# Kernel optimization log

Hardware: AMD Instinct MI355X
Metric: run time of the kernel (lower is better)

## Reference

```python
import jax, jax.numpy as jnp
import numpy as np

B = 2048        # batch
C = 4           # number of constraint matrices per sample
NRIS = 100      # physical RIS elements (theta dim)
MN = 16         # N_t * N_r
DIN = 303
DOUT = 200 + 4 * MN  # 264
THRESH_W = 10.0 ** (-120.0 / 10.0) / 1000.0  # 1e-15


def _init_linear(key, fan_in, fan_out):
    kw, _ = jax.random.split(key)
    W = jax.random.normal(kw, (fan_in, fan_out), dtype=jnp.float32) * (1.0 / np.sqrt(fan_in))
    b = jnp.zeros((fan_out,), dtype=jnp.float32)
    return W, b


def setup_inputs() -> dict:
    key = jax.random.key(0)
    ks = jax.random.split(key, 8)
    sample1 = jax.random.normal(ks[0], (B, DIN), dtype=jnp.float32)
    T_real = jax.random.normal(ks[1], (B, C, NRIS, NRIS), dtype=jnp.float32)
    T_imag = jax.random.normal(ks[2], (B, C, NRIS, NRIS), dtype=jnp.float32)
    W1, b1 = _init_linear(ks[3], DIN, 1024)
    W2, b2 = _init_linear(ks[4], 1024, 1024)
    W3, b3 = _init_linear(ks[5], 1024, 512)
    W4, b4 = _init_linear(ks[6], 512, DOUT)
    return {"sample1": sample1, "T_real": T_real, "T_imag": T_imag,
            "W1": W1, "b1": b1, "W2": W2, "b2": b2,
            "W3": W3, "b3": b3, "W4": W4, "b4": b4}


def reference(sample1, T_real, T_imag, W1, b1, W2, b2, W3, b3, W4, b4):
    # --- f1 MLP: 303 -> 1024 -> 1024 -> 512 -> 264 ---
    h = jax.nn.relu(sample1 @ W1 + b1)
    h = jax.nn.relu(h @ W2 + b2)
    h = jax.nn.relu(h @ W3 + b3)
    theta1 = h @ W4 + b4  # [B, 264]

    # --- precoder normalization: F <- F * sqrt(2 / F^H F) ---
    F1 = theta1[:, 200:200 + MN] + 1j * theta1[:, 200 + MN:200 + 2 * MN]      # [B, 16]
    F2 = theta1[:, 200 + 2 * MN:200 + 3 * MN] + 1j * theta1[:, 200 + 3 * MN:]  # [B, 16]
    F1 = F1 * jnp.sqrt(2.0 / jnp.sum(jnp.abs(F1) ** 2, axis=-1, keepdims=True))
    F2 = F2 * jnp.sqrt(2.0 / jnp.sum(jnp.abs(F2) ** 2, axis=-1, keepdims=True))

    # --- unit-modulus RIS phases ---
    theta = theta1[:, 0:NRIS] + 1j * theta1[:, NRIS:2 * NRIS]  # [B, 100]
    theta = theta / jnp.abs(theta)

    # --- ProjectRIS (batched): CCC_c = Re(theta^H (T_c / thr) theta), rescale if max > 1 ---
    T = T_real + 1j * T_imag  # [B, C, 100, 100]
    quad = jnp.einsum("bn,bcnm,bm->bc", jnp.conj(theta), T, theta)
    CCC = jnp.real(quad) / jnp.float32(THRESH_W)  # [B, C]
    mx = jnp.max(CCC, axis=1)  # [B]
    # scale = sqrt(1/mx) if mx > 1 else 1  ==  rsqrt(max(mx, 1))
    scale = jax.lax.rsqrt(jnp.maximum(mx, 1.0))
    theta_hat = theta * scale[:, None]

    # --- write back into theta1 layout ---
    out = jnp.concatenate([
        jnp.real(theta_hat), jnp.imag(theta_hat),
        jnp.real(F1), jnp.imag(F1),
        jnp.real(F2), jnp.imag(F2),
    ], axis=1)  # [B, 264]
    return out
```

## Files before the change

kernel.cpp:

```cpp
#include <hip/hip_runtime.h>
#include <math.h>

#define BATCH 2048
#define NRIS  100
#define MN    16
#define DIN   303
#define DOUT  264
#define TH1_LD 320

typedef short     bf16x8 __attribute__((ext_vector_type(8)));
typedef float     f32x4  __attribute__((ext_vector_type(4)));
typedef unsigned short u16;

__device__ __forceinline__ u16 f2bf(float x) {
    unsigned u = __float_as_uint(x);
    unsigned r = (u + 0x7fffu + ((u >> 16) & 1u)) >> 16;
    return (u16)r;
}
__device__ __forceinline__ float bf2f(u16 h) {
    return __uint_as_float(((unsigned)h) << 16);
}

__device__ __forceinline__ void gload_lds16(const void* g, void* lds) {
    __builtin_amdgcn_global_load_lds(
        (const __attribute__((address_space(1))) unsigned int*)g,
        (__attribute__((address_space(3))) unsigned int*)lds, 16, 0, 0);
}

template <int BM, int BN, bool RELU, bool SPLIT>
__global__ __launch_bounds__(256) void gemm_bf16x3(
    const u16* __restrict__ Ahi, const u16* __restrict__ Alo,
    const u16* __restrict__ Bhi, const u16* __restrict__ Blo,
    const float* __restrict__ bias, int Nb,
    float* __restrict__ Cf, u16* __restrict__ Chi, u16* __restrict__ Clo,
    int M, int N, int Kp)
{
    constexpr int WR = BM / 2, WC = BN / 2;
    constexpr int FM = WR / 16, FN = WC / 16;
    constexpr int IA = BM / 32;
    constexpr int IB = BN / 32;

    __shared__ __align__(16) short As[2][BM][64];
    __shared__ __align__(16) short Bs[2][BN][64];

    const int tid = threadIdx.x;
    const int w  = tid >> 6, l = tid & 63;
    const int lg = l >> 4, lx = l & 15, l7 = l & 7;
    const int bm = blockIdx.x * BM, bn = blockIdx.y * BN;
    const int wrow = (w >> 1) * WR, wcol = (w & 1) * WC;
    const int nt = Kp / 32;

    auto stage = [&](int k0, int buf) {
#pragma unroll
        for (int i = 0; i < IA; ++i) {
            int fi = (w * IA + i) * 64 + l;
            int r = fi >> 3, p = fi & 7, q = p ^ (r & 7);
            const u16* src = (q < 4)
                ? Ahi + (size_t)(bm + r) * Kp + k0 + q * 8
                : Alo + (size_t)(bm + r) * Kp + k0 + (q - 4) * 8;
            gload_lds16(src, &As[buf][0][0] + (size_t)(w * IA + i) * 512);
        }
#pragma unroll
        for (int i = 0; i < IB; ++i) {
            int fi = (w * IB + i) * 64 + l;
            int r = fi >> 3, p = fi & 7, q = p ^ (r & 7);
            const u16* src = (q < 4)
                ? Bhi + (size_t)(bn + r) * Kp + k0 + q * 8
                : Blo + (size_t)(bn + r) * Kp + k0 + (q - 4) * 8;
            gload_lds16(src, &Bs[buf][0][0] + (size_t)(w * IB + i) * 512);
        }
    };

    f32x4 acc[FM][FN];
#pragma unroll
    for (int i = 0; i < FM; ++i)
#pragma unroll
        for (int j = 0; j < FN; ++j) acc[i][j] = (f32x4){0.f, 0.f, 0.f, 0.f};

    stage(0, 0);
    __syncthreads();

    for (int t = 0; t < nt; ++t) {
        int cur = t & 1, nxt = cur ^ 1;
        if (t + 1 < nt) stage((t + 1) * 32, nxt);

        bf16x8 ah[FM], al[FM], bh[FN], bl[FN];
#pragma unroll
        for (int fm = 0; fm < FM; ++fm) {
            const short* base = &As[cur][wrow + fm * 16 + lx][0];
            ah[fm] = *(const bf16x8*)(base + ((lg ^ l7) << 3));
            al[fm] = *(const bf16x8*)(base + (((lg + 4) ^ l7) << 3));
        }
#pragma unroll
        for (int fn = 0; fn < FN; ++fn) {
            const short* base = &Bs[cur][wcol + fn * 16 + lx][0];
            bh[fn] = *(const bf16x8*)(base + ((lg ^ l7) << 3));
            bl[fn] = *(const bf16x8*)(base + (((lg + 4) ^ l7) << 3));
        }
#pragma unroll
        for (int fm = 0; fm < FM; ++fm)
#pragma unroll
            for (int fn = 0; fn < FN; ++fn) {
                acc[fm][fn] = __builtin_amdgcn_mfma_f32_16x16x32_bf16(
                    ah[fm], bh[fn], acc[fm][fn], 0, 0, 0);
                acc[fm][fn] = __builtin_amdgcn_mfma_f32_16x16x32_bf16(
                    ah[fm], bl[fn], acc[fm][fn], 0, 0, 0);
                acc[fm][fn] = __builtin_amdgcn_mfma_f32_16x16x32_bf16(
                    al[fm], bh[fn], acc[fm][fn], 0, 0, 0);
            }
        __syncthreads();
    }

#pragma unroll
    for (int fm = 0; fm < FM; ++fm)
#pragma unroll
        for (int fn = 0; fn < FN; ++fn) {
            int colg = bn + wcol + fn * 16 + lx;
            float bb = (colg < Nb) ? bias[colg] : 0.f;
#pragma unroll
            for (int r = 0; r < 4; ++r) {
                int rowg = bm + wrow + fm * 16 + lg * 4 + r;
                float v = acc[fm][fn][r] + bb;
                if (RELU) v = fmaxf(v, 0.f);
                if constexpr (SPLIT) {
                    u16 h = f2bf(v);
                    size_t o = (size_t)rowg * N + colg;
                    Chi[o] = h;
                    Clo[o] = f2bf(v - bf2f(h));
                } else {
                    Cf[(size_t)rowg * N + colg] = v;
                }
            }
        }
}

__global__ __launch_bounds__(256) void convtr_kernel(
    const float* __restrict__ W, u16* __restrict__ BThi, u16* __restrict__ BTlo,
    int K, int N, int Kp, int Np)
{
    __shared__ float T[64][65];
    int k0 = blockIdx.x * 64, n0 = blockIdx.y * 64;
    int c  = threadIdx.x & 63, r4 = threadIdx.x >> 6;
#pragma unroll
    for (int i = 0; i < 16; ++i) {
        int r = r4 * 16 + i;
        float v = 0.f;
        if (k0 + r < K && n0 + c < N) v = W[(size_t)(k0 + r) * N + n0 + c];
        T[r][c] = v;
    }
    __syncthreads();
#pragma unroll
    for (int i = 0; i < 16; ++i) {
        int nr = r4 * 16 + i;
        float v = T[c][nr];
        u16 h = f2bf(v);
        size_t o = (size_t)(n0 + nr) * Kp + k0 + c;
        BThi[o] = h;
        BTlo[o] = f2bf(v - bf2f(h));
    }
}

__global__ __launch_bounds__(256) void convpad_kernel(
    const float* __restrict__ X, u16* __restrict__ Hi, u16* __restrict__ Lo,
    int K, int Kp)
{
    int b = blockIdx.x;
    for (int k = threadIdx.x; k < Kp; k += 256) {
        float v = (k < K) ? X[(size_t)b * K + k] : 0.f;
        u16 h = f2bf(v);
        Hi[(size_t)b * Kp + k] = h;
        Lo[(size_t)b * Kp + k] = f2bf(v - bf2f(h));
    }
}

__global__ __launch_bounds__(128) void theta_prep_kernel(
    const float* __restrict__ th1, float* __restrict__ thU,
    float* __restrict__ out)
{
    int b   = blockIdx.x;
    int tid = threadIdx.x;
    const float* row = th1 + (size_t)b * TH1_LD;
    __shared__ float sc[2];

    if (tid == 112) {
        float s = 0.f;
        for (int j = 0; j < MN; ++j) {
            float fr = row[200 + j], fi = row[200 + MN + j];
            s += fr * fr + fi * fi;
        }
        sc[0] = sqrtf(2.f / s);
    } else if (tid == 113) {
        float s = 0.f;
        for (int j = 0; j < MN; ++j) {
            float fr = row[200 + 2 * MN + j], fi = row[200 + 3 * MN + j];
            s += fr * fr + fi * fi;
        }
        sc[1] = sqrtf(2.f / s);
    }

    if (tid < NRIS) {
        float re = row[tid], im = row[NRIS + tid];
        float r  = sqrtf(re * re + im * im);
        thU[(size_t)b * 200 + tid]        = re / r;
        thU[(size_t)b * 200 + NRIS + tid] = im / r;
    }
    __syncthreads();
    if (tid < 32) {
        int j = tid & 15, h = tid >> 4;
        out[(size_t)b * DOUT + 200 + h * MN + j]          = row[200 + h * MN + j] * sc[0];
        out[(size_t)b * DOUT + 200 + 2 * MN + h * MN + j] = row[200 + 2 * MN + h * MN + j] * sc[1];
    }
}

__global__ __launch_bounds__(256) void quadfin_kernel(
    const float* __restrict__ Tr, const float* __restrict__ Ti,
    const float* __restrict__ thU, float* __restrict__ out)
{
    int b   = blockIdx.x;
    int tid = threadIdx.x;

    __shared__ __align__(16) float sA[NRIS];
    __shared__ __align__(16) float sB[NRIS];
    if (tid < 200) {
        float v = thU[(size_t)b * 200 + tid];
        if (tid < NRIS) sA[tid] = v;
        else            sB[tid - NRIS] = v;
    }
    __syncthreads();

    const float4* R0 = (const float4*)(Tr + (size_t)b * 4 * (NRIS * NRIS));
    const float4* I0 = (const float4*)(Ti + (size_t)b * 4 * (NRIS * NRIS));

    float acc0 = 0.f, acc1 = 0.f, acc2 = 0.f, acc3 = 0.f;
    int n = tid / 25;
    int m = tid - n * 25;
    for (int j = tid; j < 2500; j += 256) {
        float an = sA[n], bn = sB[n];
        float4 am = *(const float4*)&sA[m * 4];
        float4 bm = *(const float4*)&sB[m * 4];
        float4 tR, tI;
        tR.x = an * am.x + bn * bm.x;  tI.x = bn * am.x - an * bm.x;
        tR.y = an * am.y + bn * bm.y;  tI.y = bn * am.y - an * bm.y;
        tR.z = an * am.z + bn * bm.z;  tI.z = bn * am.z - an * bm.z;
        tR.w = an * am.w + bn * bm.w;  tI.w = bn * am.w - an * bm.w;

        float4 r0 = R0[j],            i0 = I0[j];
        float4 r1 = R0[2500 + j],     i1 = I0[2500 + j];
        float4 r2 = R0[5000 + j],     i2 = I0[5000 + j];
        float4 r3 = R0[7500 + j],     i3 = I0[7500 + j];

        acc0 += r0.x * tR.x + r0.y * tR.y + r0.z * tR.z + r0.w * tR.w
              + i0.x * tI.x + i0.y * tI.y + i0.z * tI.z + i0.w * tI.w;
        acc1 += r1.x * tR.x + r1.y * tR.y + r1.z * tR.z + r1.w * tR.w
              + i1.x * tI.x + i1.y * tI.y + i1.z * tI.z + i1.w * tI.w;
        acc2 += r2.x * tR.x + r2.y * tR.y + r2.z * tR.z + r2.w * tR.w
              + i2.x * tI.x + i2.y * tI.y + i2.z * tI.z + i2.w * tI.w;
        acc3 += r3.x * tR.x + r3.y * tR.y + r3.z * tR.z + r3.w * tR.w
              + i3.x * tI.x + i3.y * tI.y + i3.z * tI.z + i3.w * tI.w;

        n += 10; m += 6;
        if (m >= 25) { m -= 25; ++n; }
    }

    int wave = tid >> 6, lane = tid & 63;
    for (int off = 32; off > 0; off >>= 1) {
        acc0 += __shfl_down(acc0, off, 64);
        acc1 += __shfl_down(acc1, off, 64);
        acc2 += __shfl_down(acc2, off, 64);
        acc3 += __shfl_down(acc3, off, 64);
    }
    __shared__ float ws4[4][4];
    if (lane == 0) {
        ws4[wave][0] = acc0; ws4[wave][1] = acc1;
        ws4[wave][2] = acc2; ws4[wave][3] = acc3;
    }
    __syncthreads();

    __shared__ float sc;
    if (tid == 0) {
        float mx = -1e30f;
#pragma unroll
        for (int c = 0; c < 4; ++c) {
            float s = ws4[0][c] + ws4[1][c] + ws4[2][c] + ws4[3][c];
            mx = fmaxf(mx, s);
        }
        mx *= 1e15f;
        sc = 1.f / sqrtf(fmaxf(mx, 1.0f));
    }
    __syncthreads();
    if (tid < NRIS) {
        out[(size_t)b * DOUT + tid]        = sA[tid] * sc;
        out[(size_t)b * DOUT + NRIS + tid] = sB[tid] * sc;
    }
}

extern "C" void kernel_launch(void* const* d_in, const int* in_sizes, int n_in,
                              void* d_out, int out_size, void* d_ws, size_t ws_size,
                              hipStream_t stream)
{
    const float* sample1 = (const float*)d_in[0];
    const float* T_real  = (const float*)d_in[1];
    const float* T_imag  = (const float*)d_in[2];
    const float* W1 = (const float*)d_in[3];
    const float* b1 = (const float*)d_in[4];
    const float* W2 = (const float*)d_in[5];
    const float* b2 = (const float*)d_in[6];
    const float* W3 = (const float*)d_in[7];
    const float* b3 = (const float*)d_in[8];
    const float* W4 = (const float*)d_in[9];
    const float* b4 = (const float*)d_in[10];
    float* out = (float*)d_out;

    char* p = (char*)d_ws;
    auto take = [&](size_t bytes) { char* q = p; p += bytes; return q; };
    u16* Shi   = (u16*)take((size_t)BATCH * 320 * 2);
    u16* Slo   = (u16*)take((size_t)BATCH * 320 * 2);
    u16* BT1hi = (u16*)take((size_t)1024 * 320 * 2);
    u16* BT1lo = (u16*)take((size_t)1024 * 320 * 2);
    u16* BT2hi = (u16*)take((size_t)1024 * 1024 * 2);
    u16* BT2lo = (u16*)take((size_t)1024 * 1024 * 2);
    u16* BT3hi = (u16*)take((size_t)512 * 1024 * 2);
    u16* BT3lo = (u16*)take((size_t)512 * 1024 * 2);
    u16* BT4hi = (u16*)take((size_t)320 * 512 * 2);
    u16* BT4lo = (u16*)take((size_t)320 * 512 * 2);
    u16* h1hi  = (u16*)take((size_t)BATCH * 1024 * 2);
    u16* h1lo  = (u16*)take((size_t)BATCH * 1024 * 2);
    u16* h2hi  = (u16*)take((size_t)BATCH * 1024 * 2);
    u16* h2lo  = (u16*)take((size_t)BATCH * 1024 * 2);
    u16* h3hi  = (u16*)take((size_t)BATCH * 512 * 2);
    u16* h3lo  = (u16*)take((size_t)BATCH * 512 * 2);
    float* th1 = (float*)take((size_t)BATCH * TH1_LD * 4);
    float* thU = (float*)take((size_t)BATCH * 200 * 4);

    dim3 blk(256);

    convpad_kernel<<<dim3(BATCH), blk, 0, stream>>>(sample1, Shi, Slo, DIN, 320);
    convtr_kernel<<<dim3(320 / 64, 1024 / 64), blk, 0, stream>>>(
        W1, BT1hi, BT1lo, DIN, 1024, 320, 1024);
    convtr_kernel<<<dim3(1024 / 64, 1024 / 64), blk, 0, stream>>>(
        W2, BT2hi, BT2lo, 1024, 1024, 1024, 1024);
    convtr_kernel<<<dim3(1024 / 64, 512 / 64), blk, 0, stream>>>(
        W3, BT3hi, BT3lo, 1024, 512, 1024, 512);
    convtr_kernel<<<dim3(512 / 64, 320 / 64), blk, 0, stream>>>(
        W4, BT4hi, BT4lo, 512, 264, 512, 320);

    gemm_bf16x3<64, 64, true, true><<<dim3(32, 16), blk, 0, stream>>>(
        Shi, Slo, BT1hi, BT1lo, b1, 1024, nullptr, h1hi, h1lo, BATCH, 1024, 320);
    gemm_bf16x3<64, 64, true, true><<<dim3(32, 16), blk, 0, stream>>>(
        h1hi, h1lo, BT2hi, BT2lo, b2, 1024, nullptr, h2hi, h2lo, BATCH, 1024, 1024);
    gemm_bf16x3<32, 64, true, true><<<dim3(64, 8), blk, 0, stream>>>(
        h2hi, h2lo, BT3hi, BT3lo, b3, 512, nullptr, h3hi, h3lo, BATCH, 512, 1024);
    gemm_bf16x3<32, 64, false, false><<<dim3(64, 5), blk, 0, stream>>>(
        h3hi, h3lo, BT4hi, BT4lo, b4, DOUT, th1, nullptr, nullptr, BATCH, TH1_LD, 512);

    theta_prep_kernel<<<dim3(BATCH), dim3(128), 0, stream>>>(th1, thU, out);
    quadfin_kernel<<<dim3(BATCH), blk, 0, stream>>>(T_real, T_imag, thU, out);
}
```

Measured before the change: 739.7 us.

## Widen GEMM K-tile, merge conversion kernels, fuse theta prep into quad kernel

```diff
diff --git a/kernel.cpp b/kernel.cpp
--- a/kernel.cpp
+++ b/kernel.cpp
@@ -37,36 +37,36 @@
 {
     constexpr int WR = BM / 2, WC = BN / 2;
     constexpr int FM = WR / 16, FN = WC / 16;
-    constexpr int IA = BM / 32;
-    constexpr int IB = BN / 32;
-
-    __shared__ __align__(16) short As[2][BM][64];
-    __shared__ __align__(16) short Bs[2][BN][64];
+    constexpr int IA = BM / 16;
+    constexpr int IB = BN / 16;
+
+    __shared__ __align__(16) short As[2][BM][128];
+    __shared__ __align__(16) short Bs[2][BN][128];
 
     const int tid = threadIdx.x;
     const int w  = tid >> 6, l = tid & 63;
-    const int lg = l >> 4, lx = l & 15, l7 = l & 7;
+    const int lg = l >> 4, lx = l & 15;
     const int bm = blockIdx.x * BM, bn = blockIdx.y * BN;
     const int wrow = (w >> 1) * WR, wcol = (w & 1) * WC;
-    const int nt = Kp / 32;
+    const int nt = Kp / 64;
 
     auto stage = [&](int k0, int buf) {
 #pragma unroll
         for (int i = 0; i < IA; ++i) {
             int fi = (w * IA + i) * 64 + l;
-            int r = fi >> 3, p = fi & 7, q = p ^ (r & 7);
-            const u16* src = (q < 4)
+            int r = fi >> 4, p = fi & 15, q = p ^ (r & 15);
+            const u16* src = (q < 8)
                 ? Ahi + (size_t)(bm + r) * Kp + k0 + q * 8
-                : Alo + (size_t)(bm + r) * Kp + k0 + (q - 4) * 8;
+                : Alo + (size_t)(bm + r) * Kp + k0 + (q - 8) * 8;
             gload_lds16(src, &As[buf][0][0] + (size_t)(w * IA + i) * 512);
         }
 #pragma unroll
         for (int i = 0; i < IB; ++i) {
             int fi = (w * IB + i) * 64 + l;
-            int r = fi >> 3, p = fi & 7, q = p ^ (r & 7);
-            const u16* src = (q < 4)
+            int r = fi >> 4, p = fi & 15, q = p ^ (r & 15);
+            const u16* src = (q < 8)
                 ? Bhi + (size_t)(bn + r) * Kp + k0 + q * 8
-                : Blo + (size_t)(bn + r) * Kp + k0 + (q - 4) * 8;
+                : Blo + (size_t)(bn + r) * Kp + k0 + (q - 8) * 8;
             gload_lds16(src, &Bs[buf][0][0] + (size_t)(w * IB + i) * 512);
         }
     };
@@ -82,32 +82,39 @@
 
     for (int t = 0; t < nt; ++t) {
         int cur = t & 1, nxt = cur ^ 1;
-        if (t + 1 < nt) stage((t + 1) * 32, nxt);
-
-        bf16x8 ah[FM], al[FM], bh[FN], bl[FN];
-#pragma unroll
-        for (int fm = 0; fm < FM; ++fm) {
-            const short* base = &As[cur][wrow + fm * 16 + lx][0];
-            ah[fm] = *(const bf16x8*)(base + ((lg ^ l7) << 3));
-            al[fm] = *(const bf16x8*)(base + (((lg + 4) ^ l7) << 3));
-        }
-#pragma unroll
-        for (int fn = 0; fn < FN; ++fn) {
-            const short* base = &Bs[cur][wcol + fn * 16 + lx][0];
-            bh[fn] = *(const bf16x8*)(base + ((lg ^ l7) << 3));
-            bl[fn] = *(const bf16x8*)(base + (((lg + 4) ^ l7) << 3));
-        }
-#pragma unroll
-        for (int fm = 0; fm < FM; ++fm)
+        if (t + 1 < nt) stage((t + 1) * 64, nxt);
+
+#pragma unroll
+        for (int s = 0; s < 2; ++s) {
+            bf16x8 ah[FM], al[FM], bh[FN], bl[FN];
+#pragma unroll
+            for (int fm = 0; fm < FM; ++fm) {
+                int row = wrow + fm * 16 + lx;
+                const short* base = &As[cur][row][0];
+                int r15 = row & 15;
+                ah[fm] = *(const bf16x8*)(base + (((s * 4 + lg) ^ r15) << 3));
+                al[fm] = *(const bf16x8*)(base + (((8 + s * 4 + lg) ^ r15) << 3));
+            }
 #pragma unroll
             for (int fn = 0; fn < FN; ++fn) {
-                acc[fm][fn] = __builtin_amdgcn_mfma_f32_16x16x32_bf16(
-                    ah[fm], bh[fn], acc[fm][fn], 0, 0, 0);
-                acc[fm][fn] = __builtin_amdgcn_mfma_f32_16x16x32_bf16(
-                    ah[fm], bl[fn], acc[fm][fn], 0, 0, 0);
-                acc[fm][fn] = __builtin_amdgcn_mfma_f32_16x16x32_bf16(
-                    al[fm], bh[fn], acc[fm][fn], 0, 0, 0);
+                int row = wcol + fn * 16 + lx;
+                const short* base = &Bs[cur][row][0];
+                int r15 = row & 15;
+                bh[fn] = *(const bf16x8*)(base + (((s * 4 + lg) ^ r15) << 3));
+                bl[fn] = *(const bf16x8*)(base + (((8 + s * 4 + lg) ^ r15) << 3));
             }
+#pragma unroll
+            for (int fm = 0; fm < FM; ++fm)
+#pragma unroll
+                for (int fn = 0; fn < FN; ++fn) {
+                    acc[fm][fn] = __builtin_amdgcn_mfma_f32_16x16x32_bf16(
+                        ah[fm], bh[fn], acc[fm][fn], 0, 0, 0);
+                    acc[fm][fn] = __builtin_amdgcn_mfma_f32_16x16x32_bf16(
+                        ah[fm], bl[fn], acc[fm][fn], 0, 0, 0);
+                    acc[fm][fn] = __builtin_amdgcn_mfma_f32_16x16x32_bf16(
+                        al[fm], bh[fn], acc[fm][fn], 0, 0, 0);
+                }
+        }
         __syncthreads();
     }
 
@@ -134,12 +141,35 @@
         }
 }
 
-__global__ __launch_bounds__(256) void convtr_kernel(
-    const float* __restrict__ W, u16* __restrict__ BThi, u16* __restrict__ BTlo,
-    int K, int N, int Kp, int Np)
+__global__ __launch_bounds__(256) void convert_all_kernel(
+    const float* __restrict__ s1,
+    const float* __restrict__ W1, const float* __restrict__ W2,
+    const float* __restrict__ W3, const float* __restrict__ W4,
+    u16* __restrict__ Shi, u16* __restrict__ Slo,
+    u16* __restrict__ B1h, u16* __restrict__ B1l,
+    u16* __restrict__ B2h, u16* __restrict__ B2l,
+    u16* __restrict__ B3h, u16* __restrict__ B3l,
+    u16* __restrict__ B4h, u16* __restrict__ B4l)
 {
+    int bid = blockIdx.x;
+    if (bid >= 504) {
+        int b = bid - 504;
+        for (int k = threadIdx.x; k < 320; k += 256) {
+            float v = (k < DIN) ? s1[(size_t)b * DIN + k] : 0.f;
+            u16 h = f2bf(v);
+            Shi[(size_t)b * 320 + k] = h;
+            Slo[(size_t)b * 320 + k] = f2bf(v - bf2f(h));
+        }
+        return;
+    }
+    const float* W; u16 *Hh, *Ll; int K, N, Kp, gw;
+    if (bid < 80)       {            W = W1; Hh = B1h; Ll = B1l; K = DIN;  N = 1024; Kp = 320;  gw = 5;  }
+    else if (bid < 336) { bid -= 80;  W = W2; Hh = B2h; Ll = B2l; K = 1024; N = 1024; Kp = 1024; gw = 16; }
+    else if (bid < 464) { bid -= 336; W = W3; Hh = B3h; Ll = B3l; K = 1024; N = 512;  Kp = 1024; gw = 16; }
+    else                { bid -= 464; W = W4; Hh = B4h; Ll = B4l; K = 512;  N = DOUT; Kp = 512;  gw = 8;  }
+
     __shared__ float T[64][65];
-    int k0 = blockIdx.x * 64, n0 = blockIdx.y * 64;
+    int k0 = (bid % gw) * 64, n0 = (bid / gw) * 64;
     int c  = threadIdx.x & 63, r4 = threadIdx.x >> 6;
 #pragma unroll
     for (int i = 0; i < 16; ++i) {
@@ -155,78 +185,49 @@
         float v = T[c][nr];
         u16 h = f2bf(v);
         size_t o = (size_t)(n0 + nr) * Kp + k0 + c;
-        BThi[o] = h;
-        BTlo[o] = f2bf(v - bf2f(h));
-    }
-}
-
-__global__ __launch_bounds__(256) void convpad_kernel(
-    const float* __restrict__ X, u16* __restrict__ Hi, u16* __restrict__ Lo,
-    int K, int Kp)
-{
-    int b = blockIdx.x;
-    for (int k = threadIdx.x; k < Kp; k += 256) {
-        float v = (k < K) ? X[(size_t)b * K + k] : 0.f;
-        u16 h = f2bf(v);
-        Hi[(size_t)b * Kp + k] = h;
-        Lo[(size_t)b * Kp + k] = f2bf(v - bf2f(h));
-    }
-}
-
-__global__ __launch_bounds__(128) void theta_prep_kernel(
-    const float* __restrict__ th1, float* __restrict__ thU,
-    float* __restrict__ out)
+        Hh[o] = h;
+        Ll[o] = f2bf(v - bf2f(h));
+    }
+}
+
+__global__ __launch_bounds__(256) void quadfin_kernel(
+    const float* __restrict__ Tr, const float* __restrict__ Ti,
+    const float* __restrict__ th1, float* __restrict__ out)
 {
     int b   = blockIdx.x;
     int tid = threadIdx.x;
     const float* row = th1 + (size_t)b * TH1_LD;
-    __shared__ float sc[2];
-
-    if (tid == 112) {
+
+    __shared__ __align__(16) float sA[NRIS];
+    __shared__ __align__(16) float sB[NRIS];
+    __shared__ float sc2[2];
+
+    if (tid < NRIS) {
+        float re = row[tid], im = row[NRIS + tid];
+        float rr = sqrtf(re * re + im * im);
+        sA[tid] = re / rr;
+        sB[tid] = im / rr;
+    } else if (tid == 112) {
         float s = 0.f;
         for (int j = 0; j < MN; ++j) {
             float fr = row[200 + j], fi = row[200 + MN + j];
             s += fr * fr + fi * fi;
         }
-        sc[0] = sqrtf(2.f / s);
+        sc2[0] = sqrtf(2.f / s);
     } else if (tid == 113) {
         float s = 0.f;
         for (int j = 0; j < MN; ++j) {
             float fr = row[200 + 2 * MN + j], fi = row[200 + 3 * MN + j];
             s += fr * fr + fi * fi;
         }
-        sc[1] = sqrtf(2.f / s);
-    }
-
-    if (tid < NRIS) {
-        float re = row[tid], im = row[NRIS + tid];
-        float r  = sqrtf(re * re + im * im);
-        thU[(size_t)b * 200 + tid]        = re / r;
-        thU[(size_t)b * 200 + NRIS + tid] = im / r;
+        sc2[1] = sqrtf(2.f / s);
     }
     __syncthreads();
     if (tid < 32) {
         int j = tid & 15, h = tid >> 4;
-        out[(size_t)b * DOUT + 200 + h * MN + j]          = row[200 + h * MN + j] * sc[0];
-        out[(size_t)b * DOUT + 200 + 2 * MN + h * MN + j] = row[200 + 2 * MN + h * MN + j] * sc[1];
-    }
-}
-
-__global__ __launch_bounds__(256) void quadfin_kernel(
-    const float* __restrict__ Tr, const float* __restrict__ Ti,
-    const float* __restrict__ thU, float* __restrict__ out)
-{
-    int b   = blockIdx.x;
-    int tid = threadIdx.x;
-
-    __shared__ __align__(16) float sA[NRIS];
-    __shared__ __align__(16) float sB[NRIS];
-    if (tid < 200) {
-        float v = thU[(size_t)b * 200 + tid];
-        if (tid < NRIS) sA[tid] = v;
-        else            sB[tid - NRIS] = v;
-    }
-    __syncthreads();
+        out[(size_t)b * DOUT + 200 + h * MN + j]          = row[200 + h * MN + j] * sc2[0];
+        out[(size_t)b * DOUT + 200 + 2 * MN + h * MN + j] = row[200 + 2 * MN + h * MN + j] * sc2[1];
+    }
 
     const float4* R0 = (const float4*)(Tr + (size_t)b * 4 * (NRIS * NRIS));
     const float4* I0 = (const float4*)(Ti + (size_t)b * 4 * (NRIS * NRIS));
@@ -330,19 +331,12 @@
     u16* h3hi  = (u16*)take((size_t)BATCH * 512 * 2);
     u16* h3lo  = (u16*)take((size_t)BATCH * 512 * 2);
     float* th1 = (float*)take((size_t)BATCH * TH1_LD * 4);
-    float* thU = (float*)take((size_t)BATCH * 200 * 4);
 
     dim3 blk(256);
 
-    convpad_kernel<<<dim3(BATCH), blk, 0, stream>>>(sample1, Shi, Slo, DIN, 320);
-    convtr_kernel<<<dim3(320 / 64, 1024 / 64), blk, 0, stream>>>(
-        W1, BT1hi, BT1lo, DIN, 1024, 320, 1024);
-    convtr_kernel<<<dim3(1024 / 64, 1024 / 64), blk, 0, stream>>>(
-        W2, BT2hi, BT2lo, 1024, 1024, 1024, 1024);
-    convtr_kernel<<<dim3(1024 / 64, 512 / 64), blk, 0, stream>>>(
-        W3, BT3hi, BT3lo, 1024, 512, 1024, 512);
-    convtr_kernel<<<dim3(512 / 64, 320 / 64), blk, 0, stream>>>(
-        W4, BT4hi, BT4lo, 512, 264, 512, 320);
+    convert_all_kernel<<<dim3(2552), blk, 0, stream>>>(
+        sample1, W1, W2, W3, W4, Shi, Slo,
+        BT1hi, BT1lo, BT2hi, BT2lo, BT3hi, BT3lo, BT4hi, BT4lo);
 
     gemm_bf16x3<64, 64, true, true><<<dim3(32, 16), blk, 0, stream>>>(
         Shi, Slo, BT1hi, BT1lo, b1, 1024, nullptr, h1hi, h1lo, BATCH, 1024, 320);
@@ -353,6 +347,5 @@
     gemm_bf16x3<32, 64, false, false><<<dim3(64, 5), blk, 0, stream>>>(
         h3hi, h3lo, BT4hi, BT4lo, b4, DOUT, th1, nullptr, nullptr, BATCH, TH1_LD, 512);
 
-    theta_prep_kernel<<<dim3(BATCH), dim3(128), 0, stream>>>(th1, thU, out);
-    quadfin_kernel<<<dim3(BATCH), blk, 0, stream>>>(T_real, T_imag, thU, out);
-}
+    quadfin_kernel<<<dim3(BATCH), blk, 0, stream>>>(T_real, T_imag, th1, out);
+}
```

New measurement: 693.0 us. 1.07x faster.
